# Performance work log

Measured on AMD Instinct MI355X. Metric: run time of the kernel, lower is better.

The kernel has to match this reference:

```python
import jax, jax.numpy as jnp
import numpy as np

LAYER_SIZES = [256, 256, 256, 128]
MAX_PATHS = 100
BATCH = 16


def setup_inputs() -> dict:
    key = jax.random.key(0)
    ks = jax.random.split(key, 20)
    d = {}
    d["x"] = jax.random.normal(ks[0], (BATCH, LAYER_SIZES[0]), dtype=jnp.float32)
    # PathPreservingLayer weights W_l: [out, in]
    for l in range(3):
        fi, fo = LAYER_SIZES[l], LAYER_SIZES[l + 1]
        d[f"W{l}"] = jax.random.normal(ks[1 + l], (fo, fi), dtype=jnp.float32) / np.sqrt(fi)
        # quality scorer for layer l: Linear(fo,32) -> ReLU -> Linear(32,1)
        kk = jax.random.split(ks[4 + l], 4)
        d[f"s{l}_w1"] = jax.random.normal(kk[0], (32, fo), dtype=jnp.float32) / np.sqrt(fo)
        d[f"s{l}_b1"] = jnp.zeros((32,), dtype=jnp.float32)
        d[f"s{l}_w2"] = jax.random.normal(kk[1], (1, 32), dtype=jnp.float32) / np.sqrt(32.0)
        d[f"s{l}_b2"] = jnp.zeros((1,), dtype=jnp.float32)
    return d


def _path_layer(data, W):
    # data: [B, Fin, P]; W: [Fout, Fin]
    # path-preserving expansion: new[b, j, p*Fin + i] = W[j, i] * data[b, i, p]
    B, I, P = data.shape
    O = W.shape[0]
    out = jnp.einsum("oi,bip->bopi", W, data)  # [B, O, P, I]
    return out.reshape(B, O, P * I)


def _score(data, w1, b1, w2, b2):
    # data: [B, F, P] -> scores [B, P] via tiny MLP over feature dim per path
    t = jnp.swapaxes(data, 1, 2)  # [B, P, F]
    h = jax.nn.relu(jnp.einsum("bpf,hf->bph", t, w1) + b1)
    return (jnp.einsum("bph,oh->bpo", h, w2) + b2)[..., 0]


def _prune(data, scores, keep):
    _, idx = jax.lax.top_k(scores, keep)  # [B, keep]
    return jnp.take_along_axis(data, idx[:, None, :], axis=-1)


def reference(x, W0, W1, W2,
              s0_w1, s0_b1, s0_w2, s0_b2,
              s1_w1, s1_b1, s1_w2, s1_b2,
              s2_w1, s2_b1, s2_w2, s2_b2):
    Ws = [W0, W1, W2]
    scorers = [(s0_w1, s0_b1, s0_w2, s0_b2),
               (s1_w1, s1_b1, s1_w2, s1_b2),
               (s2_w1, s2_b1, s2_w2, s2_b2)]
    data = x[..., None]  # [B, F0, 1]
    n = len(Ws)
    for i in range(n):
        data = _path_layer(data, Ws[i])
        if data.shape[-1] > MAX_PATHS:
            sc = _score(data, *scorers[i])
            data = _prune(data, sc, MAX_PATHS)
        if i < n - 1:
            data = jnp.tanh(data)
    # quality-weighted output with the last scorer
    w = jax.nn.softmax(_score(data, *scorers[-1]), axis=-1)  # [B, P]
    return jnp.sum(data * w[:, None, :], axis=-1)  # [B, F_last]
```

## Files before the change

kernel.cpp:

```cpp
#include <hip/hip_runtime.h>
#include <math.h>

#define NT 1024
#define KSEL 100
#define NW0 8
#define HPAD 260
#define CCAP 2048

#define OFF_CT   0
#define OFF_W0T  24576
#define OFF_W1T  90112
#define OFF_W2T  155648
#define WS_FLOATS 188416

__device__ __forceinline__ unsigned fkey(float f) {
  unsigned u = __float_as_uint(f);
  return (u & 0x80000000u) ? ~u : (u | 0x80000000u);
}
__device__ __forceinline__ float unfkey(unsigned k) {
  return __uint_as_float((k & 0x80000000u) ? (k & 0x7FFFFFFFu) : ~k);
}
__device__ __forceinline__ unsigned long long lower_mask(int lane) {
  return lane ? (~0ull >> (64 - lane)) : 0ull;
}

__device__ __forceinline__ float fast_tanhf(float x) {
  float ax = fabsf(x);
  float e = __expf(-2.f * ax);
  float r = (1.f - e) * __builtin_amdgcn_rcpf(1.f + e);
  r = (ax > 10.f) ? 1.f : r;
  return copysignf(r, x);
}

__device__ __forceinline__ void scan_step(const unsigned* hb, int ncopies, int lane,
                                          int& krem, unsigned& prefix) {
  const int l4 = lane << 2;
  unsigned h0 = 0, h1 = 0, h2 = 0, h3 = 0;
  #pragma unroll 2
  for (int k = 0; k < ncopies; ++k) {
    const uint4 v = *(const uint4*)&hb[k * HPAD + l4];
    h0 += v.x; h1 += v.y; h2 += v.z; h3 += v.w;
  }
  unsigned csum = h0 + h1 + h2 + h3;
  unsigned S = csum;
  #pragma unroll
  for (int off = 1; off < 64; off <<= 1) {
    unsigned v = __shfl_down(S, off, 64);
    if (lane + off < 64) S += v;
  }
  unsigned tail = S - csum;
  unsigned s3 = tail + h3;
  unsigned s2 = s3 + h2;
  unsigned s1 = s2 + h1;
  unsigned s0v = s1 + h0;
  int ld = -1; unsigned sfx = 0, hd = 0;
  if      ((int)s3  >= krem) { ld = l4 + 3; sfx = s3;  hd = h3; }
  else if ((int)s2  >= krem) { ld = l4 + 2; sfx = s2;  hd = h2; }
  else if ((int)s1  >= krem) { ld = l4 + 1; sfx = s1;  hd = h1; }
  else if ((int)s0v >= krem) { ld = l4 + 0; sfx = s0v; hd = h0; }
  int gd = ld;
  #pragma unroll
  for (int off = 32; off >= 1; off >>= 1) {
    int v = __shfl_down(gd, off, 64);
    if (lane + off < 64) gd = (v > gd) ? v : gd;
  }
  gd = __shfl(gd, 0, 64);
  unsigned osfx = __shfl(sfx, gd >> 2, 64);
  unsigned ohd  = __shfl(hd,  gd >> 2, 64);
  krem -= (int)(osfx - ohd);
  prefix = (prefix << 8) | (unsigned)gd;
}

__global__ __launch_bounds__(256) void pqn_precompute(
    const float* __restrict__ W0, const float* __restrict__ W1, const float* __restrict__ W2,
    const float* __restrict__ s0w1, const float* __restrict__ s1w1, const float* __restrict__ s2w1,
    float* __restrict__ ws)
{
  __shared__ float tile[64][65];
  const int bx = blockIdx.x, t = threadIdx.x;
  if (bx < 96) {
    int id = bx * 256 + t;
    int l = id >> 13, r = id & 8191;
    int h = r >> 8, i = r & 255;
    const float* W  = (l == 0) ? W0 : (l == 1) ? W1 : W2;
    const float* w1 = (l == 0) ? s0w1 : (l == 1) ? s1w1 : s2w1;
    float acc = 0.f;
    if (l == 2) {
      #pragma unroll 32
      for (int j = 0; j < 128; ++j) acc = fmaf(w1[h * 128 + j], W[j * 256 + i], acc);
    } else {
      #pragma unroll 32
      for (int j = 0; j < 256; ++j) acc = fmaf(w1[h * 256 + j], W[j * 256 + i], acc);
    }
    ws[OFF_CT + l * 8192 + h * 256 + i] = acc;
  } else {
    int tb = bx - 96;
    const float* W; float* WT; int R, tbl;
    if (tb < 16)      { W = W0; WT = ws + OFF_W0T; R = 256; tbl = tb; }
    else if (tb < 32) { W = W1; WT = ws + OFF_W1T; R = 256; tbl = tb - 16; }
    else              { W = W2; WT = ws + OFF_W2T; R = 128; tbl = tb - 32; }
    int tr = tbl >> 2, tc = tbl & 3;
    int c = t & 63, r0 = t >> 6;
    #pragma unroll
    for (int k = 0; k < 16; ++k) {
      int r = r0 + (k << 2);
      tile[r][c] = W[(tr * 64 + r) * 256 + tc * 64 + c];
    }
    __syncthreads();
    int r2 = t & 63;
    #pragma unroll
    for (int k = 0; k < 16; ++k) {
      int c2 = r0 + (k << 2);
      WT[(tc * 64 + c2) * R + tr * 64 + r2] = tile[r2][c2];
    }
  }
}

__device__ __forceinline__ float slow_c(const float* __restrict__ w1,
                                        const float* __restrict__ W,
                                        int Fout, int h, int i) {
  float c = 0.f;
  for (int j = 0; j < Fout; ++j) c = fmaf(w1[h * Fout + j], W[j * 256 + i], c);
  return c;
}

__global__ __launch_bounds__(NT) void pqn_main(
    const float* __restrict__ x,
    const float* __restrict__ W0, const float* __restrict__ W1, const float* __restrict__ W2,
    const float* __restrict__ s0w1, const float* __restrict__ s1w1, const float* __restrict__ s2w1,
    const float* __restrict__ s0b1, const float* __restrict__ s1b1, const float* __restrict__ s2b1,
    const float* __restrict__ s0w2, const float* __restrict__ s1w2, const float* __restrict__ s2w2,
    const float* __restrict__ s0b2, const float* __restrict__ s1b2, const float* __restrict__ s2b2,
    const float* __restrict__ wsr,
    float* __restrict__ out)
{
  __shared__ __align__(16) unsigned keyLds[25 * NT];
  __shared__ __align__(16) unsigned hist0[NW0 * HPAD];
  __shared__ __align__(16) unsigned histP[6 * HPAD];
  __shared__ unsigned candK[CCAP]; __shared__ int candE[CCAP];
  __shared__ __align__(16) float As[2][256];
  __shared__ __align__(16) float Bs[2][256];
  __shared__ int   path_col[KSEL]; __shared__ float path_t[KSEL];
  __shared__ int   sel_col[KSEL];  __shared__ float sel_s[KSEL]; __shared__ float sel_sc[KSEL];
  __shared__ unsigned tieq[128];
  __shared__ int nsel_s, ntie_s, ncand_s;
  __shared__ int bz_sh[3];
  __shared__ float wts[KSEL];
  __shared__ float partial[8][128];

  const int b = blockIdx.x;
  const int t = threadIdx.x;
  const int lane = t & 63;
  const int w = t >> 6;
  const bool useWs = (wsr != nullptr);
  const float* Ctg = useWs ? (wsr + OFF_CT) : nullptr;
  const float* W0T = useWs ? (wsr + OFF_W0T) : nullptr;
  const float* W1T = useWs ? (wsr + OFF_W1T) : nullptr;
  const float* W2T = useWs ? (wsr + OFF_W2T) : nullptr;

  if (t >= 256) {
    int l = 1 + ((t - 256) >> 8), i = t & 255;
    if (l <= 2) {
      const float* w2 = (l == 1) ? s1w2 : s2w2;
      float a = 0.f, bn = 0.f;
      if (useWs) {
        const float* ct = Ctg + l * 8192;
        #pragma unroll
        for (int h = 0; h < 32; ++h) {
          float c = ct[h * 256 + i];
          float wc = w2[h] * c;
          if (c > 0.f) a += wc; else if (c < 0.f) bn += wc;
        }
      } else {
        const float* W  = (l == 1) ? W1 : W2;
        const float* w1 = (l == 1) ? s1w1 : s2w1;
        const int Fout = (l == 2) ? 128 : 256;
        for (int h = 0; h < 32; ++h) {
          float c = slow_c(w1, W, Fout, h, i);
          float wc = w2[h] * c;
          if (c > 0.f) a += wc; else if (c < 0.f) bn += wc;
        }
      }
      As[l - 1][i] = a; Bs[l - 1][i] = bn;
    }
  } else if (w == 0) {
    {
      float v0 = (lane < 32) ? s0b1[lane] : 0.f;
      float v1 = (lane < 32) ? s1b1[lane] : 0.f;
      float v2 = (lane < 32) ? s2b1[lane] : 0.f;
      bz_sh[0] = (__ballot(v0 != 0.f) == 0ull);
      bz_sh[1] = (__ballot(v1 != 0.f) == 0ull);
      bz_sh[2] = (__ballot(v2 != 0.f) == 0ull);
    }
    const float b2v = s0b2[0];
    const float4 xv4 = *(const float4*)(x + b * 256 + lane * 4);
    const float xv[4] = {xv4.x, xv4.y, xv4.z, xv4.w};
    float vq[4] = {b2v, b2v, b2v, b2v};
    if (useWs) {
      #pragma unroll 8
      for (int h = 0; h < 32; ++h) {
        const float4 c4 = *(const float4*)(Ctg + h * 256 + 4 * lane);
        const float w2h = s0w2[h], b1h = s0b1[h];
        vq[0] += w2h * fmaxf(fmaf(xv[0], c4.x, b1h), 0.f);
        vq[1] += w2h * fmaxf(fmaf(xv[1], c4.y, b1h), 0.f);
        vq[2] += w2h * fmaxf(fmaf(xv[2], c4.z, b1h), 0.f);
        vq[3] += w2h * fmaxf(fmaf(xv[3], c4.w, b1h), 0.f);
      }
    } else {
      for (int h = 0; h < 32; ++h) {
        const float w2h = s0w2[h], b1h = s0b1[h];
        #pragma unroll
        for (int q = 0; q < 4; ++q) {
          float c = slow_c(s0w1, W0, 256, h, 4 * lane + q);
          vq[q] += w2h * fmaxf(fmaf(xv[q], c, b1h), 0.f);
        }
      }
    }
    unsigned kq[4];
    #pragma unroll
    for (int q = 0; q < 4; ++q) kq[q] = fkey(vq[q]);

    int krem = KSEL; unsigned prefix = 0u;
    #pragma unroll
    for (int pass = 0; pass < 4; ++pass) {
      unsigned* hw = (pass == 0) ? hist0 : (histP + (pass - 1) * 2 * HPAD);
      const int l4 = lane << 2;
      hw[l4] = 0u; hw[l4 + 1] = 0u; hw[l4 + 2] = 0u; hw[l4 + 3] = 0u;
      const int shift = 24 - 8 * pass;
      #pragma unroll
      for (int q = 0; q < 4; ++q) {
        bool cand = (pass == 0) || ((kq[q] >> (shift + 8)) == prefix);
        if (cand) atomicAdd(&hw[(kq[q] >> shift) & 255u], 1u);
      }
      scan_step(hw, 1, lane, krem, prefix);
    }
    const unsigned T = prefix;
    int total = 0, ttot = 0;
    #pragma unroll
    for (int q = 0; q < 4; ++q) {
      int e = 4 * lane + q;
      bool sel = kq[q] > T;
      unsigned long long m = __ballot(sel);
      if (sel) {
        int slot = total + (int)__popcll(m & lower_mask(lane));
        path_col[slot] = e; path_t[slot] = xv[q];
      }
      total += (int)__popcll(m);
      bool tie = (kq[q] == T);
      unsigned long long tm = __ballot(tie);
      if (tie) {
        int ts = ttot + (int)__popcll(tm & lower_mask(lane));
        if (ts < 128) tieq[ts] = (unsigned)e;
      }
      ttot += (int)__popcll(tm);
    }
    if (lane == 0) {
      int m = ttot > 128 ? 128 : ttot;
      for (int a2 = 1; a2 < m; ++a2) {
        unsigned v = tieq[a2]; int c = a2 - 1;
        while (c >= 0 && tieq[c] > v) { tieq[c + 1] = tieq[c]; --c; }
        tieq[c + 1] = v;
      }
    }
    const int kt = KSEL - total;
    if (lane < kt) {
      int e = (int)tieq[lane];
      path_col[total + lane] = e; path_t[total + lane] = x[b * 256 + e];
    }
  }
  __syncthreads();

  for (int l = 1; l < 3; ++l) {
    const float* w1 = (l == 1) ? s1w1 : s2w1;
    const float* b1 = (l == 1) ? s1b1 : s2b1;
    const float* w2 = (l == 1) ? s1w2 : s2w2;
    const float  b2v = (l == 1) ? s1b2[0] : s2b2[0];
    const float* Wl = (l == 1) ? W1 : W2;
    const float* Wprev = (l == 1) ? W0 : W1;
    const float* WTprev = (l == 1) ? W0T : W1T;
    const int Fout = (l == 2) ? 128 : 256;
    const bool bz = (bz_sh[l] != 0);
    const float* ctp = useWs ? (Ctg + l * 8192) : nullptr;

    const int i = t & 255;
    const int pq = t >> 8;
    const float Ai = As[l - 1][i], Bi = Bs[l - 1][i];
    unsigned* histw0 = hist0 + (w >> 1) * HPAD;
    {
      const int l4 = lane << 2;
      histw0[l4] = 0u; histw0[l4 + 1] = 0u; histw0[l4 + 2] = 0u; histw0[l4 + 3] = 0u;
    }
    for (int id = t; id < 6 * HPAD; id += NT) histP[id] = 0u;
    if (t == 0) { nsel_s = 0; ntie_s = 0; ncand_s = 0; }
    unsigned runD = 0x100u; unsigned runC = 0u;
    if (useWs && bz) {
      #pragma unroll
      for (int g = 0; g < 25; g += 8) {
        float wv[8], tv[8];
        #pragma unroll
        for (int jj = 0; jj < 8; ++jj) {
          if (g + jj < 25) {
            int p = pq + ((g + jj) << 2);
            tv[jj] = path_t[p];
            wv[jj] = WTprev[(path_col[p] << 8) + i];
          }
        }
        #pragma unroll
        for (int jj = 0; jj < 8; ++jj) {
          if (g + jj < 25) {
            float s = fast_tanhf(wv[jj] * tv[jj]);
            float v = s * (s > 0.f ? Ai : Bi) + b2v;
            unsigned k = fkey(v);
            keyLds[(g + jj) * NT + t] = k;
            unsigned d = k >> 24;
            if (d == runD) ++runC;
            else { if (runC) atomicAdd(&histw0[runD], runC); runD = d; runC = 1u; }
          }
        }
      }
    } else {
      #pragma unroll
      for (int g = 0; g < 25; g += 4) {
        float wv[4];
        #pragma unroll
        for (int jj = 0; jj < 4; ++jj) {
          if (g + jj < 25) {
            int p = pq + ((g + jj) << 2);
            wv[jj] = useWs ? WTprev[(path_col[p] << 8) + i]
                           : Wprev[i * 256 + path_col[p]];
          }
        }
        #pragma unroll
        for (int jj = 0; jj < 4; ++jj) {
          if (g + jj < 25) {
            int p = pq + ((g + jj) << 2);
            float s = fast_tanhf(wv[jj] * path_t[p]);
            float v;
            if (bz) v = s * (s > 0.f ? Ai : Bi) + b2v;
            else {
              v = b2v;
              for (int h = 0; h < 32; ++h) {
                float c = useWs ? ctp[h * 256 + i] : slow_c(w1, Wl, Fout, h, i);
                v += w2[h] * fmaxf(fmaf(s, c, b1[h]), 0.f);
              }
            }
            unsigned k = fkey(v);
            keyLds[(g + jj) * NT + t] = k;
            unsigned d = k >> 24;
            if (d == runD) ++runC;
            else { if (runC) atomicAdd(&histw0[runD], runC); runD = d; runC = 1u; }
          }
        }
      }
    }
    if (runC) atomicAdd(&histw0[runD], runC);

    __syncthreads();
    int krem = KSEL; unsigned prefix = 0u;
    scan_step(hist0, NW0, lane, krem, prefix);

    {
      unsigned* hn = histP + (w & 1) * HPAD;
      #pragma unroll
      for (int j = 0; j < 25; ++j) {
        unsigned k = keyLds[j * NT + t];
        if ((k >> 24) == prefix) atomicAdd(&hn[(k >> 16) & 255u], 1u);
      }
    }
    __syncthreads();
    scan_step(histP, 2, lane, krem, prefix);

    {
      unsigned* hn = histP + 2 * HPAD + (w & 1) * HPAD;
      #pragma unroll
      for (int j = 0; j < 25; ++j) {
        unsigned k = keyLds[j * NT + t];
        unsigned p16 = k >> 16;
        if (p16 > prefix) {
          int slot = atomicAdd(&nsel_s, 1);
          int e = j * NT + t; int p = e >> 8;
          float wq = useWs ? WTprev[(path_col[p] << 8) + i] : Wprev[i * 256 + path_col[p]];
          sel_col[slot] = i; sel_s[slot] = fast_tanhf(wq * path_t[p]); sel_sc[slot] = unfkey(k);
        } else if (p16 == prefix) {
          int ci = atomicAdd(&ncand_s, 1);
          if (ci < CCAP) { candK[ci] = k; candE[ci] = j * NT + t; }
          atomicAdd(&hn[(k >> 8) & 255u], 1u);
        }
      }
    }
    __syncthreads();
    scan_step(histP + 2 * HPAD, 2, lane, krem, prefix);
    const int ncand = ncand_s;
    const bool ovf = (ncand > CCAP);

    {
      unsigned* hn = histP + 4 * HPAD + (w & 1) * HPAD;
      if (!ovf) {
        for (int idx = t; idx < ncand; idx += NT) {
          unsigned k = candK[idx];
          if ((k >> 8) == prefix) atomicAdd(&hn[k & 255u], 1u);
        }
      } else {
        #pragma unroll
        for (int j = 0; j < 25; ++j) {
          unsigned k = keyLds[j * NT + t];
          if ((k >> 8) == prefix) atomicAdd(&hn[k & 255u], 1u);
        }
      }
    }
    __syncthreads();
    scan_step(histP + 4 * HPAD, 2, lane, krem, prefix);
    const unsigned T = prefix;

    if (!ovf) {
      for (int idx = t; idx < ncand; idx += NT) {
        unsigned k = candK[idx];
        if (k > T) {
          int e = candE[idx];
          int slot = atomicAdd(&nsel_s, 1);
          int ii = e & 255, p = e >> 8;
          float wq = useWs ? WTprev[(path_col[p] << 8) + ii] : Wprev[ii * 256 + path_col[p]];
          sel_col[slot] = ii; sel_s[slot] = fast_tanhf(wq * path_t[p]); sel_sc[slot] = unfkey(k);
        } else if (k == T) {
          int tp = atomicAdd(&ntie_s, 1);
          if (tp < 128) tieq[tp] = (unsigned)candE[idx];
        }
      }
    } else {
      #pragma unroll
      for (int j = 0; j < 25; ++j) {
        unsigned k = keyLds[j * NT + t];
        if ((k >> 16) == (T >> 16)) {
          int e = j * NT + t;
          if (k > T) {
            int slot = atomicAdd(&nsel_s, 1);
            int p = e >> 8;
            float wq = useWs ? WTprev[(path_col[p] << 8) + i] : Wprev[i * 256 + path_col[p]];
            sel_col[slot] = i; sel_s[slot] = fast_tanhf(wq * path_t[p]); sel_sc[slot] = unfkey(k);
          } else if (k == T) {
            int tp = atomicAdd(&ntie_s, 1);
            if (tp < 128) tieq[tp] = (unsigned)e;
          }
        }
      }
    }
    __syncthreads();

    if (w == 0) {
      const int G = nsel_s;
      const int kt = KSEL - G;
      if (lane == 0 && kt > 1) {
        int m = ntie_s > 128 ? 128 : ntie_s;
        for (int a2 = 1; a2 < m; ++a2) {
          unsigned v = tieq[a2]; int c = a2 - 1;
          while (c >= 0 && tieq[c] > v) { tieq[c + 1] = tieq[c]; --c; }
          tieq[c + 1] = v;
        }
      }
      if (lane < kt) {
        int e = (int)tieq[lane];
        int ii = e & 255, p = e >> 8;
        float wq = useWs ? WTprev[(path_col[p] << 8) + ii] : Wprev[ii * 256 + path_col[p]];
        sel_col[G + lane] = ii;
        sel_s[G + lane] = fast_tanhf(wq * path_t[p]);
        sel_sc[G + lane] = unfkey(T);
      }
      if (l < 2) {
        if (lane < 64) {
          path_col[lane] = sel_col[lane]; path_t[lane] = sel_s[lane];
          if (lane < 36) { path_col[64 + lane] = sel_col[64 + lane]; path_t[64 + lane] = sel_s[64 + lane]; }
        }
      }
    }
    __syncthreads();
  }

  if (w == 0) {
    float s1v = sel_sc[lane];
    float s2v = (lane < 36) ? sel_sc[64 + lane] : -INFINITY;
    float m = fmaxf(s1v, s2v);
    #pragma unroll
    for (int off = 32; off >= 1; off >>= 1) m = fmaxf(m, __shfl_xor(m, off, 64));
    float e1 = expf(s1v - m);
    float e2 = (lane < 36) ? expf(s2v - m) : 0.f;
    float sv = e1 + e2;
    #pragma unroll
    for (int off = 32; off >= 1; off >>= 1) sv += __shfl_xor(sv, off, 64);
    wts[lane] = e1 * sel_s[lane] / sv;
    if (lane < 36) wts[64 + lane] = e2 * sel_s[64 + lane] / sv;
  }
  __syncthreads();
  {
    const int chunk = w >> 1, half = w & 1;
    const int o = half * 64 + lane;
    const int pb = chunk * 13;
    const int pe = (pb + 13 < KSEL) ? pb + 13 : KSEL;
    float acc = 0.f;
    for (int p = pb; p < pe; ++p) {
      float wq = useWs ? W2T[sel_col[p] * 128 + o] : W2[o * 256 + sel_col[p]];
      acc = fmaf(wq, wts[p], acc);
    }
    partial[chunk][o] = acc;
  }
  __syncthreads();
  if (t < 128) {
    float acc = 0.f;
    #pragma unroll
    for (int c = 0; c < 8; ++c) acc += partial[c][t];
    out[b * 128 + t] = acc;
  }
}

extern "C" void kernel_launch(void* const* d_in, const int* in_sizes, int n_in,
                              void* d_out, int out_size, void* d_ws, size_t ws_size,
                              hipStream_t stream) {
  const float* x    = (const float*)d_in[0];
  const float* W0   = (const float*)d_in[1];
  const float* s0w1 = (const float*)d_in[2];
  const float* s0b1 = (const float*)d_in[3];
  const float* s0w2 = (const float*)d_in[4];
  const float* s0b2 = (const float*)d_in[5];
  const float* W1   = (const float*)d_in[6];
  const float* s1w1 = (const float*)d_in[7];
  const float* s1b1 = (const float*)d_in[8];
  const float* s1w2 = (const float*)d_in[9];
  const float* s1b2 = (const float*)d_in[10];
  const float* W2   = (const float*)d_in[11];
  const float* s2w1 = (const float*)d_in[12];
  const float* s2b1 = (const float*)d_in[13];
  const float* s2w2 = (const float*)d_in[14];
  const float* s2b2 = (const float*)d_in[15];
  float* out = (float*)d_out;
  float* ws  = (float*)d_ws;

  const bool haveWs = ws_size >= (size_t)WS_FLOATS * sizeof(float);
  const float* wsr = nullptr;
  if (haveWs) {
    pqn_precompute<<<136, 256, 0, stream>>>(W0, W1, W2, s0w1, s1w1, s2w1, ws);
    wsr = ws;
  }
  pqn_main<<<16, NT, 0, stream>>>(x, W0, W1, W2,
                                  s0w1, s1w1, s2w1,
                                  s0b1, s1b1, s2b1,
                                  s0w2, s1w2, s2w2,
                                  s0b2, s1b2, s2b2,
                                  wsr, out);
}
```

Before: 140.5 us.

## Replace last two radix-select passes with direct candidate ranking; split precompute accumulators

Top-k selection now stops radix passes after the second byte. Remaining candidates are ranked directly by pairwise comparison against all other candidates, which removes two histogram/scan/barrier rounds on the common path. The full radix path is kept only for candidate-buffer overflow. The precompute dot product also uses four independent accumulators to break the FMA dependency chain. Risks are an O(n^2) ranking cost when many candidates exist, and a confusing tie fix-up block that rewrites sel_sc with odd expressions.

```diff
diff --git a/kernel.cpp b/kernel.cpp
--- a/kernel.cpp
+++ b/kernel.cpp
@@ -84,15 +84,25 @@
     int h = r >> 8, i = r & 255;
     const float* W  = (l == 0) ? W0 : (l == 1) ? W1 : W2;
     const float* w1 = (l == 0) ? s0w1 : (l == 1) ? s1w1 : s2w1;
-    float acc = 0.f;
+    float a0 = 0.f, a1 = 0.f, a2 = 0.f, a3 = 0.f;
     if (l == 2) {
-      #pragma unroll 32
-      for (int j = 0; j < 128; ++j) acc = fmaf(w1[h * 128 + j], W[j * 256 + i], acc);
+      #pragma unroll 8
+      for (int j = 0; j < 128; j += 4) {
+        a0 = fmaf(w1[h * 128 + j    ], W[(j    ) * 256 + i], a0);
+        a1 = fmaf(w1[h * 128 + j + 1], W[(j + 1) * 256 + i], a1);
+        a2 = fmaf(w1[h * 128 + j + 2], W[(j + 2) * 256 + i], a2);
+        a3 = fmaf(w1[h * 128 + j + 3], W[(j + 3) * 256 + i], a3);
+      }
     } else {
-      #pragma unroll 32
-      for (int j = 0; j < 256; ++j) acc = fmaf(w1[h * 256 + j], W[j * 256 + i], acc);
-    }
-    ws[OFF_CT + l * 8192 + h * 256 + i] = acc;
+      #pragma unroll 8
+      for (int j = 0; j < 256; j += 4) {
+        a0 = fmaf(w1[h * 256 + j    ], W[(j    ) * 256 + i], a0);
+        a1 = fmaf(w1[h * 256 + j + 1], W[(j + 1) * 256 + i], a1);
+        a2 = fmaf(w1[h * 256 + j + 2], W[(j + 2) * 256 + i], a2);
+        a3 = fmaf(w1[h * 256 + j + 3], W[(j + 3) * 256 + i], a3);
+      }
+    }
+    ws[OFF_CT + l * 8192 + h * 256 + i] = (a0 + a1) + (a2 + a3);
   } else {
     int tb = bx - 96;
     const float* W; float* WT; int R, tbl;
@@ -290,7 +300,7 @@
       const int l4 = lane << 2;
       histw0[l4] = 0u; histw0[l4 + 1] = 0u; histw0[l4 + 2] = 0u; histw0[l4 + 3] = 0u;
     }
-    for (int id = t; id < 6 * HPAD; id += NT) histP[id] = 0u;
+    for (int id = t; id < 2 * HPAD; id += NT) histP[id] = 0u;
     if (t == 0) { nsel_s = 0; ntie_s = 0; ncand_s = 0; }
     unsigned runD = 0x100u; unsigned runC = 0u;
     if (useWs && bz) {
@@ -370,63 +380,62 @@
     __syncthreads();
     scan_step(histP, 2, lane, krem, prefix);
 
-    {
-      unsigned* hn = histP + 2 * HPAD + (w & 1) * HPAD;
-      #pragma unroll
-      for (int j = 0; j < 25; ++j) {
-        unsigned k = keyLds[j * NT + t];
-        unsigned p16 = k >> 16;
-        if (p16 > prefix) {
-          int slot = atomicAdd(&nsel_s, 1);
-          int e = j * NT + t; int p = e >> 8;
-          float wq = useWs ? WTprev[(path_col[p] << 8) + i] : Wprev[i * 256 + path_col[p]];
-          sel_col[slot] = i; sel_s[slot] = fast_tanhf(wq * path_t[p]); sel_sc[slot] = unfkey(k);
-        } else if (p16 == prefix) {
-          int ci = atomicAdd(&ncand_s, 1);
-          if (ci < CCAP) { candK[ci] = k; candE[ci] = j * NT + t; }
-          atomicAdd(&hn[(k >> 8) & 255u], 1u);
-        }
+    #pragma unroll
+    for (int j = 0; j < 25; ++j) {
+      unsigned k = keyLds[j * NT + t];
+      unsigned p16 = k >> 16;
+      if (p16 > prefix) {
+        int slot = atomicAdd(&nsel_s, 1);
+        int e = j * NT + t; int p = e >> 8;
+        float wq = useWs ? WTprev[(path_col[p] << 8) + i] : Wprev[i * 256 + path_col[p]];
+        sel_col[slot] = i; sel_s[slot] = fast_tanhf(wq * path_t[p]); sel_sc[slot] = unfkey(k);
+      } else if (p16 == prefix) {
+        int ci = atomicAdd(&ncand_s, 1);
+        if (ci < CCAP) { candK[ci] = k; candE[ci] = j * NT + t; }
       }
     }
     __syncthreads();
-    scan_step(histP + 2 * HPAD, 2, lane, krem, prefix);
     const int ncand = ncand_s;
-    const bool ovf = (ncand > CCAP);
-
-    {
-      unsigned* hn = histP + 4 * HPAD + (w & 1) * HPAD;
-      if (!ovf) {
-        for (int idx = t; idx < ncand; idx += NT) {
-          unsigned k = candK[idx];
-          if ((k >> 8) == prefix) atomicAdd(&hn[k & 255u], 1u);
-        }
-      } else {
-        #pragma unroll
-        for (int j = 0; j < 25; ++j) {
-          unsigned k = keyLds[j * NT + t];
-          if ((k >> 8) == prefix) atomicAdd(&hn[k & 255u], 1u);
-        }
-      }
-    }
-    __syncthreads();
-    scan_step(histP + 4 * HPAD, 2, lane, krem, prefix);
-    const unsigned T = prefix;
-
-    if (!ovf) {
+
+    if (ncand <= CCAP) {
       for (int idx = t; idx < ncand; idx += NT) {
-        unsigned k = candK[idx];
-        if (k > T) {
-          int e = candE[idx];
+        unsigned k = candK[idx]; int e = candE[idx];
+        int rnk = 0;
+        for (int j2 = 0; j2 < ncand; ++j2) {
+          unsigned kj = candK[j2];
+          rnk += (kj > k) || (kj == k && candE[j2] < e);
+        }
+        if (rnk < krem) {
           int slot = atomicAdd(&nsel_s, 1);
           int ii = e & 255, p = e >> 8;
           float wq = useWs ? WTprev[(path_col[p] << 8) + ii] : Wprev[ii * 256 + path_col[p]];
           sel_col[slot] = ii; sel_s[slot] = fast_tanhf(wq * path_t[p]); sel_sc[slot] = unfkey(k);
-        } else if (k == T) {
-          int tp = atomicAdd(&ntie_s, 1);
-          if (tp < 128) tieq[tp] = (unsigned)candE[idx];
         }
       }
     } else {
+      for (int id = 2 * HPAD + t; id < 6 * HPAD; id += NT) histP[id] = 0u;
+      __syncthreads();
+      {
+        unsigned* hn = histP + 2 * HPAD + (w & 1) * HPAD;
+        #pragma unroll
+        for (int j = 0; j < 25; ++j) {
+          unsigned k = keyLds[j * NT + t];
+          if ((k >> 16) == prefix) atomicAdd(&hn[(k >> 8) & 255u], 1u);
+        }
+      }
+      __syncthreads();
+      scan_step(histP + 2 * HPAD, 2, lane, krem, prefix);
+      {
+        unsigned* hn = histP + 4 * HPAD + (w & 1) * HPAD;
+        #pragma unroll
+        for (int j = 0; j < 25; ++j) {
+          unsigned k = keyLds[j * NT + t];
+          if ((k >> 8) == prefix) atomicAdd(&hn[k & 255u], 1u);
+        }
+      }
+      __syncthreads();
+      scan_step(histP + 4 * HPAD, 2, lane, krem, prefix);
+      const unsigned T = prefix;
       #pragma unroll
       for (int j = 0; j < 25; ++j) {
         unsigned k = keyLds[j * NT + t];
@@ -463,7 +472,12 @@
         float wq = useWs ? WTprev[(path_col[p] << 8) + ii] : Wprev[ii * 256 + path_col[p]];
         sel_col[G + lane] = ii;
         sel_s[G + lane] = fast_tanhf(wq * path_t[p]);
-        sel_sc[G + lane] = unfkey(T);
+        sel_sc[G + lane] = unfkey(keyLds[0] == 0 ? 0u : 0u) , sel_sc[G + lane] = unfkey(fkey(sel_s[G + lane]));
+      }
+      if (lane < kt) {
+        int e = (int)tieq[lane];
+        unsigned k = keyLds[(e / NT) * NT + (e % NT)];
+        sel_sc[G + lane] = unfkey(k);
       }
       if (l < 2) {
         if (lane < 64) {
```

After: 143.4 us. 1.02x slower.
